# Optimization experiments

Measured on AMD Instinct MI355X. Metric: run time of the kernel, lower is better.

Reference implementation:

```python
import jax, jax.numpy as jnp
import numpy as np

SINK_MAX = 128  # max materialized sink tokens (atten_sink counts are < 64)
NEG_INF = -1e30


def _gather_paged(kv, block_table, pos):
    """Gather tokens from a paged KV cache.
    kv: [num_blocks, block_size, 2, Hkv, D]; block_table: [B, max_blocks] int;
    pos: [B, L] token positions (assumed clipped to valid range).
    Returns [B, L, 2, Hkv, D]."""
    nb, bs = kv.shape[0], kv.shape[1]
    B = pos.shape[0]
    blk = jnp.take_along_axis(block_table, pos // bs, axis=1)  # [B, L]
    flat_idx = blk * bs + pos % bs                              # [B, L]
    kv_flat = kv.reshape(nb * bs, *kv.shape[2:])
    return kv_flat[flat_idx]


def setup_inputs() -> dict:
    key = jax.random.key(0)
    ks = jax.random.split(key, 6)
    B, H, Hkv, D = 32, 32, 4, 128
    NB, BS, NBC = 2048, 128, 512
    MAX_BLK, MAX_CBLK, NSEL = 64, 16, 256
    query = jax.random.normal(ks[0], (B, H, D), dtype=jnp.float32)
    ori_kv = jax.random.normal(ks[1], (NB, BS, 2, Hkv, D), dtype=jnp.float32)
    cmp_kv = jax.random.normal(ks[2], (NBC, BS, 2, Hkv, D), dtype=jnp.float32)
    ori_block_table = (jnp.arange(B * MAX_BLK) % NB).reshape(B, MAX_BLK).astype(jnp.int32)
    cmp_block_table = (jnp.arange(B * MAX_CBLK) % NBC).reshape(B, MAX_CBLK).astype(jnp.int32)
    atten_sink = jax.random.randint(ks[3], (B,), 1, 64, dtype=jnp.int32)
    seqused_kv = jax.random.randint(ks[4], (B,), 4096, 8192, dtype=jnp.int32)
    cmp_sparse_indices = jnp.sort(jax.random.randint(ks[5], (B, NSEL), 0, 1024, dtype=jnp.int32), axis=1)
    return {
        'query_npu': query,
        'q_act_seqs_npu': jnp.ones((B,), dtype=jnp.int32),
        'ori_kv_npu': ori_kv,
        'cmp_kv_npu': cmp_kv,
        'ori_block_table_npu': ori_block_table,
        'cmp_block_table_npu': cmp_block_table,
        'atten_sink_npu': atten_sink,
        'seqused_kv_npu': seqused_kv,
        'cmp_sparse_indices_npu': cmp_sparse_indices,
        'softmax_scale': float(1.0 / np.sqrt(D)),
        'win_size': 512,
        'cmp_ratio': 4,
    }


def reference(query_npu, q_act_seqs_npu, ori_kv_npu, cmp_kv_npu,
              ori_block_table_npu, cmp_block_table_npu, atten_sink_npu,
              seqused_kv_npu, cmp_sparse_indices_npu, softmax_scale,
              win_size, cmp_ratio):
    B, H, D = query_npu.shape
    Hkv = ori_kv_npu.shape[3]
    G = H // Hkv
    bs = ori_kv_npu.shape[1]
    seq = seqused_kv_npu[:, None].astype(jnp.int32)          # [B,1]
    sink = atten_sink_npu[:, None].astype(jnp.int32)         # [B,1]

    # --- sink tokens (first atten_sink tokens of the original cache) ---
    pos_s = jnp.broadcast_to(jnp.arange(SINK_MAX, dtype=jnp.int32)[None, :], (B, SINK_MAX))
    mask_s = (pos_s < sink) & (pos_s < seq)
    kv_s = _gather_paged(ori_kv_npu, ori_block_table_npu, jnp.clip(pos_s, 0))

    # --- sliding window (last win_size original tokens, excluding sink overlap) ---
    pos_w = seq - win_size + jnp.arange(win_size, dtype=jnp.int32)[None, :]
    mask_w = (pos_w >= 0) & (pos_w >= sink)
    kv_w = _gather_paged(ori_kv_npu, ori_block_table_npu, jnp.clip(pos_w, 0))

    # --- sparse-selected compressed tokens ---
    cmp_len = seq // cmp_ratio
    idx_c = cmp_sparse_indices_npu.astype(jnp.int32)         # [B, NSEL]
    mask_c = idx_c < cmp_len
    kv_c = _gather_paged(cmp_kv_npu, cmp_block_table_npu, jnp.clip(idx_c, 0))

    # --- combine all KV sources: [B, L, 2, Hkv, D] ---
    kv = jnp.concatenate([kv_s, kv_w, kv_c], axis=1)
    k, v = kv[:, :, 0], kv[:, :, 1]                           # [B, L, Hkv, D]
    mask = jnp.concatenate([mask_s, mask_w, mask_c], axis=1)  # [B, L]

    # --- GQA attention: heads grouped per kv head ---
    q = query_npu.reshape(B, Hkv, G, D)
    logits = jnp.einsum('bkgd,blkd->bkgl', q, k) * softmax_scale
    logits = jnp.where(mask[:, None, None, :], logits, NEG_INF)
    p = jax.nn.softmax(logits, axis=-1)
    out = jnp.einsum('bkgl,blkd->bkgd', p, v)
    return out.reshape(B, H, D)
```

## Files before the change

kernel.cpp:

```cpp
#include <hip/hip_runtime.h>

constexpr int B_    = 32;
constexpr int H_    = 32;
constexpr int HKV_  = 4;
constexpr int G_    = 8;
constexpr int D_    = 128;
constexpr int BS_   = 128;
constexpr int MAXBLK_  = 64;
constexpr int MAXCBLK_ = 16;
constexpr int NSEL_    = 256;
constexpr int SINKMAX_ = 128;
constexpr int WIN_     = 512;
constexpr int P_       = 8;
constexpr float MSHIFT = 24.0f;

template <int CTRL>
__device__ __forceinline__ float dpp_mov(float x) {
  return __int_as_float(__builtin_amdgcn_update_dpp(
      0, __float_as_int(x), CTRL, 0xF, 0xF, true));
}
constexpr int DPP_XOR1 = 0xB1;
constexpr int DPP_XOR2 = 0x4E;
constexpr int DPP_XOR8 = 0x128;
template <int PATT>
__device__ __forceinline__ float swz_add(float x) {
  return x + __int_as_float(
      __builtin_amdgcn_ds_swizzle(__float_as_int(x), PATT));
}

__global__ __launch_bounds__(256, 4) void sfa_partial_kernel(
    const float* __restrict__ q,
    const float* __restrict__ ori_kv,
    const float* __restrict__ cmp_kv,
    const int*   __restrict__ ori_bt,
    const int*   __restrict__ cmp_bt,
    const int*   __restrict__ sinkp,
    const int*   __restrict__ seqp,
    const int*   __restrict__ selp,
    const float* __restrict__ scalep,
    const int*   __restrict__ ratiop,
    float* __restrict__ o_out,
    float* __restrict__ s_out)
{
  const int part = blockIdx.x;
  const int kh   = blockIdx.y;
  const int b    = blockIdx.z;
  const int tid  = threadIdx.x;
  const int grp  = tid >> 5;
  const int j    = tid & 31;
  const int wave = tid >> 6;
  const int lane = tid & 63;
  const int h    = ((j & 1) << 2) | (j & 2) | ((j >> 3) & 1);
  const bool wr8 = ((j & 20) == 0);

  const float scale = scalep[0];
  const int ratio   = ratiop[0];
  const int seq     = seqp[b];
  const int sink    = sinkp[b];
  const int cmp_len = seq / ratio;

  const int sbt0 = ori_bt[b * MAXBLK_];
  int wbase = seq - WIN_; if (wbase < 0) wbase = 0;
  const int w0 = wbase >> 7;
  auto obt = [&](int k) { int w = w0 + k; if (w > MAXBLK_ - 1) w = MAXBLK_ - 1;
                          return ori_bt[b * MAXBLK_ + w]; };
  const int wb0 = obt(0), wb1 = obt(1), wb2 = obt(2), wb3 = obt(3), wb4 = obt(4);
  const int cb0 = cmp_bt[b * MAXCBLK_ + 0], cb1 = cmp_bt[b * MAXCBLK_ + 1];
  const int cb2 = cmp_bt[b * MAXCBLK_ + 2], cb3 = cmp_bt[b * MAXCBLK_ + 3];
  const int cb4 = cmp_bt[b * MAXCBLK_ + 4], cb5 = cmp_bt[b * MAXCBLK_ + 5];
  const int cb6 = cmp_bt[b * MAXCBLK_ + 6], cb7 = cmp_bt[b * MAXCBLK_ + 7];

  float4 qf[G_];
  const float* qb = q + ((size_t)b * H_ + (size_t)kh * G_) * D_ + 4 * j;
#pragma unroll
  for (int g = 0; g < G_; ++g) qf[g] = *(const float4*)(qb + g * D_);

  float  s_acc = 0.f;
  float4 oacc[G_];
#pragma unroll
  for (int m = 0; m < G_; ++m) oacc[m] = make_float4(0.f, 0.f, 0.f, 0.f);

  int s_end = sink; if (s_end < 0) s_end = 0; if (s_end > SINKMAX_) s_end = SINKMAX_;
  const int sB0 = s_end;
  const int sC0 = s_end + WIN_;
  const int L   = s_end + WIN_ + NSEL_;
  const int chunk = (L + P_ - 1) / P_;
  const int lo = part * chunk;
  int hi = lo + chunk; if (hi > L) hi = L;
  const int cf = sC0 + (((lo + grp) - sC0) & 7);
  const int sel_l = selp[b * NSEL_ + (cf - sC0) + 8 * j];

  auto process = [&](const float4 kf, const float4 vf, const float msk) {
    float lg[G_];
#pragma unroll
    for (int g = 0; g < G_; ++g)
      lg[g] = qf[g].x * kf.x + qf[g].y * kf.y + qf[g].z * kf.z + qf[g].w * kf.w;
    const bool p0 = j & 1, p1 = j & 2, p3 = j & 8;
    float s4[4];
#pragma unroll
    for (int i4 = 0; i4 < 4; ++i4) {
      const float keep = p0 ? lg[4 + i4] : lg[i4];
      const float send = p0 ? lg[i4]     : lg[4 + i4];
      s4[i4] = keep + dpp_mov<DPP_XOR1>(send);
    }
    float s2[2];
#pragma unroll
    for (int i2 = 0; i2 < 2; ++i2) {
      const float keep = p1 ? s4[2 + i2] : s4[i2];
      const float send = p1 ? s4[i2]     : s4[2 + i2];
      s2[i2] = keep + dpp_mov<DPP_XOR2>(send);
    }
    const float keep = p3 ? s2[1] : s2[0];
    const float send = p3 ? s2[0] : s2[1];
    float v1 = keep + dpp_mov<DPP_XOR8>(send);
    v1 = swz_add<0x101F>(v1);
    v1 = swz_add<0x401F>(v1);
    const float e = __expf(fminf(fmaf(v1, scale, -MSHIFT), 80.f)) * msk;
    s_acc += e;
    const float pm1 = dpp_mov<DPP_XOR8>(e);
    const float pm2 = dpp_mov<DPP_XOR2>(e);
    const float pm3 = dpp_mov<DPP_XOR2>(pm1);
    const float pm4 = dpp_mov<DPP_XOR1>(e);
    const float pm5 = dpp_mov<DPP_XOR1>(pm1);
    const float pm6 = dpp_mov<DPP_XOR1>(pm2);
    const float pm7 = dpp_mov<DPP_XOR1>(pm3);
    oacc[0].x += e   * vf.x; oacc[0].y += e   * vf.y; oacc[0].z += e   * vf.z; oacc[0].w += e   * vf.w;
    oacc[1].x += pm1 * vf.x; oacc[1].y += pm1 * vf.y; oacc[1].z += pm1 * vf.z; oacc[1].w += pm1 * vf.w;
    oacc[2].x += pm2 * vf.x; oacc[2].y += pm2 * vf.y; oacc[2].z += pm2 * vf.z; oacc[2].w += pm2 * vf.w;
    oacc[3].x += pm3 * vf.x; oacc[3].y += pm3 * vf.y; oacc[3].z += pm3 * vf.z; oacc[3].w += pm3 * vf.w;
    oacc[4].x += pm4 * vf.x; oacc[4].y += pm4 * vf.y; oacc[4].z += pm4 * vf.z; oacc[4].w += pm4 * vf.w;
    oacc[5].x += pm5 * vf.x; oacc[5].y += pm5 * vf.y; oacc[5].z += pm5 * vf.z; oacc[5].w += pm5 * vf.w;
    oacc[6].x += pm6 * vf.x; oacc[6].y += pm6 * vf.y; oacc[6].z += pm6 * vf.z; oacc[6].w += pm6 * vf.w;
    oacc[7].x += pm7 * vf.x; oacc[7].y += pm7 * vf.y; oacc[7].z += pm7 * vf.z; oacc[7].w += pm7 * vf.w;
  };

#define SEG_LOOP(S0X, S1X, ADDR_CODE)                                          \
  {                                                                            \
    const int s0q = (S0X), s1q = (S1X);                                        \
    int iq = s0q + ((lo + grp - s0q) & 7);                                     \
    if (iq < s1q) {                                                            \
      const float* kbC; float mC;                                              \
      { const int ti = iq; const float* akb; float amsk; ADDR_CODE;            \
        kbC = akb; mC = amsk; }                                                \
      float4 kfC = *(const float4*)(kbC + 4 * j);                              \
      float4 vfC = *(const float4*)(kbC + HKV_ * D_ + 4 * j);                  \
      for (; iq < s1q; iq += 8) {                                              \
        int inq = iq + 8; if (inq >= s1q) inq = s1q - 1;                       \
        const float* kbN; float mN;                                            \
        { const int ti = inq; const float* akb; float amsk; ADDR_CODE;         \
          kbN = akb; mN = amsk; }                                              \
        const float4 kfN = *(const float4*)(kbN + 4 * j);                      \
        const float4 vfN = *(const float4*)(kbN + HKV_ * D_ + 4 * j);          \
        process(kfC, vfC, mC);                                                 \
        kfC = kfN; vfC = vfN; mC = mN;                                         \
      }                                                                        \
    }                                                                          \
  }

  SEG_LOOP(lo, (hi < sB0 ? hi : sB0), {
    amsk = (ti < seq) ? 1.f : 0.f;
    akb = ori_kv + (((size_t)(sbt0 * BS_ + ti)) << 10) + kh * D_;
  });

  SEG_LOOP((lo > sB0 ? lo : sB0), (hi < sC0 ? hi : sC0), {
    const int pos = seq - WIN_ + (ti - sB0);
    amsk = (pos >= 0 && pos >= sink) ? 1.f : 0.f;
    const int pc = pos > 0 ? pos : 0;
    const int wi = (pc >> 7) - w0;
    int blk = wb0;
    blk = (wi == 1) ? wb1 : blk; blk = (wi == 2) ? wb2 : blk;
    blk = (wi == 3) ? wb3 : blk; blk = (wi == 4) ? wb4 : blk;
    akb = ori_kv + (((size_t)(blk * BS_ + (pc & (BS_ - 1)))) << 10) + kh * D_;
  });

  SEG_LOOP((lo > sC0 ? lo : sC0), hi, {
    int mI = (ti - cf) >> 3; mI = mI < 0 ? 0 : (mI > 31 ? 31 : mI);
    const int idx = __shfl(sel_l, mI, 32);
    amsk = (idx < cmp_len) ? 1.f : 0.f;
    const int pc = idx > 0 ? idx : 0;
    const int ci = pc >> 7;
    int blk = cb0;
    blk = (ci == 1) ? cb1 : blk; blk = (ci == 2) ? cb2 : blk;
    blk = (ci == 3) ? cb3 : blk; blk = (ci == 4) ? cb4 : blk;
    blk = (ci == 5) ? cb5 : blk; blk = (ci == 6) ? cb6 : blk;
    blk = (ci == 7) ? cb7 : blk;
    akb = cmp_kv + (((size_t)(blk * BS_ + (pc & (BS_ - 1)))) << 10) + kh * D_;
  });
#undef SEG_LOOP

  s_acc += __shfl_xor(s_acc, 32, 64);
  float* of = reinterpret_cast<float*>(oacc);
#pragma unroll
  for (int t = 0; t < 32; ++t) of[t] += __shfl_xor(of[t], 32, 64);

  __shared__ float lds_o[4][G_][D_];
  __shared__ float lds_s[4][G_];
  if (lane < 32) {
#pragma unroll
    for (int m = 0; m < G_; ++m)
      *(float4*)&lds_o[wave][h ^ m][4 * j] = oacc[m];
    if (wr8) lds_s[wave][h] = s_acc;
  }
  __syncthreads();

#pragma unroll
  for (int e = tid; e < G_ * D_; e += 256) {
    const int g = e >> 7, d = e & (D_ - 1);
    const float num = lds_o[0][g][d] + lds_o[1][g][d] + lds_o[2][g][d] + lds_o[3][g][d];
    o_out[(((size_t)(b * HKV_ + kh) * P_ + part) * G_ + g) * D_ + d] = num;
  }
  if (tid < G_) {
    s_out[((size_t)(b * HKV_ + kh) * P_ + part) * G_ + tid] =
        lds_s[0][tid] + lds_s[1][tid] + lds_s[2][tid] + lds_s[3][tid];
  }
}

__global__ __launch_bounds__(256) void sfa_combine_kernel(
    const float* __restrict__ op, const float* __restrict__ sp,
    float* __restrict__ out)
{
  const int idx = blockIdx.x * 256 + threadIdx.x;
  const int d  = idx & (D_ - 1);
  const int hh = (idx >> 7) & (H_ - 1);
  const int b  = idx >> 12;
  const int kh = hh >> 3, g = hh & 7;
  float num = 0.f, den = 0.f;
#pragma unroll
  for (int p = 0; p < P_; ++p) {
    num += op[(((size_t)(b * HKV_ + kh) * P_ + p) * G_ + g) * D_ + d];
    den += sp[((size_t)(b * HKV_ + kh) * P_ + p) * G_ + g];
  }
  out[idx] = num / den;
}

extern "C" void kernel_launch(void* const* d_in, const int* in_sizes, int n_in,
                              void* d_out, int out_size, void* d_ws, size_t ws_size,
                              hipStream_t stream) {
  const float* q      = (const float*)d_in[0];
  const float* ori_kv = (const float*)d_in[2];
  const float* cmp_kv = (const float*)d_in[3];
  const int*   ori_bt = (const int*)d_in[4];
  const int*   cmp_bt = (const int*)d_in[5];
  const int*   sinkp  = (const int*)d_in[6];
  const int*   seqp   = (const int*)d_in[7];
  const int*   selp   = (const int*)d_in[8];
  const float* scalep = (const float*)d_in[9];
  const int*   ratiop = (const int*)d_in[11];
  float* out = (float*)d_out;

  float* op = (float*)d_ws;
  float* sp = op + (size_t)P_ * B_ * HKV_ * G_ * D_;

  sfa_partial_kernel<<<dim3(P_, HKV_, B_), 256, 0, stream>>>(
      q, ori_kv, cmp_kv, ori_bt, cmp_bt, sinkp, seqp, selp, scalep, ratiop,
      op, sp);
  sfa_combine_kernel<<<(B_ * H_ * D_) / 256, 256, 0, stream>>>(op, sp, out);
}
```

Baseline: 26.49 us.

## Map one token per full wave with float2 lanes, 512-thread blocks, two-deep prefetch

Restructures the partial kernel so each 64-lane wave handles one token with each lane covering two D elements, instead of 32-lane half-waves covering four. Blocks grow to 512 threads (8 waves) and the split factor drops from 8 to 6 partitions. The load loop now double-buffers two tokens ahead to hide gather latency. This cuts per-thread registers and the cross-half reduction, but adds an extra cross-half shuffle per token and an 8-way LDS reduction.

```diff
diff --git a/kernel.cpp b/kernel.cpp
--- a/kernel.cpp
+++ b/kernel.cpp
@@ -11,7 +11,7 @@
 constexpr int NSEL_    = 256;
 constexpr int SINKMAX_ = 128;
 constexpr int WIN_     = 512;
-constexpr int P_       = 8;
+constexpr int P_       = 6;
 constexpr float MSHIFT = 24.0f;
 
 template <int CTRL>
@@ -28,7 +28,7 @@
       __builtin_amdgcn_ds_swizzle(__float_as_int(x), PATT));
 }
 
-__global__ __launch_bounds__(256, 4) void sfa_partial_kernel(
+__global__ __launch_bounds__(512, 6) void sfa_partial_kernel(
     const float* __restrict__ q,
     const float* __restrict__ ori_kv,
     const float* __restrict__ cmp_kv,
@@ -42,16 +42,16 @@
     float* __restrict__ o_out,
     float* __restrict__ s_out)
 {
+  __shared__ float lds_o[8][G_][D_];
+  __shared__ float lds_s[8][G_];
+
   const int part = blockIdx.x;
   const int kh   = blockIdx.y;
   const int b    = blockIdx.z;
   const int tid  = threadIdx.x;
-  const int grp  = tid >> 5;
-  const int j    = tid & 31;
-  const int wave = tid >> 6;
-  const int lane = tid & 63;
+  const int w    = tid >> 6;
+  const int j    = tid & 63;
   const int h    = ((j & 1) << 2) | (j & 2) | ((j >> 3) & 1);
-  const bool wr8 = ((j & 20) == 0);
 
   const float scale = scalep[0];
   const int ratio   = ratiop[0];
@@ -62,23 +62,13 @@
   const int sbt0 = ori_bt[b * MAXBLK_];
   int wbase = seq - WIN_; if (wbase < 0) wbase = 0;
   const int w0 = wbase >> 7;
-  auto obt = [&](int k) { int w = w0 + k; if (w > MAXBLK_ - 1) w = MAXBLK_ - 1;
-                          return ori_bt[b * MAXBLK_ + w]; };
+  auto obt = [&](int k) { int ww = w0 + k; if (ww > MAXBLK_ - 1) ww = MAXBLK_ - 1;
+                          return ori_bt[b * MAXBLK_ + ww]; };
   const int wb0 = obt(0), wb1 = obt(1), wb2 = obt(2), wb3 = obt(3), wb4 = obt(4);
   const int cb0 = cmp_bt[b * MAXCBLK_ + 0], cb1 = cmp_bt[b * MAXCBLK_ + 1];
   const int cb2 = cmp_bt[b * MAXCBLK_ + 2], cb3 = cmp_bt[b * MAXCBLK_ + 3];
   const int cb4 = cmp_bt[b * MAXCBLK_ + 4], cb5 = cmp_bt[b * MAXCBLK_ + 5];
   const int cb6 = cmp_bt[b * MAXCBLK_ + 6], cb7 = cmp_bt[b * MAXCBLK_ + 7];
-
-  float4 qf[G_];
-  const float* qb = q + ((size_t)b * H_ + (size_t)kh * G_) * D_ + 4 * j;
-#pragma unroll
-  for (int g = 0; g < G_; ++g) qf[g] = *(const float4*)(qb + g * D_);
-
-  float  s_acc = 0.f;
-  float4 oacc[G_];
-#pragma unroll
-  for (int m = 0; m < G_; ++m) oacc[m] = make_float4(0.f, 0.f, 0.f, 0.f);
 
   int s_end = sink; if (s_end < 0) s_end = 0; if (s_end > SINKMAX_) s_end = SINKMAX_;
   const int sB0 = s_end;
@@ -87,14 +77,25 @@
   const int chunk = (L + P_ - 1) / P_;
   const int lo = part * chunk;
   int hi = lo + chunk; if (hi > L) hi = L;
-  const int cf = sC0 + (((lo + grp) - sC0) & 7);
-  const int sel_l = selp[b * NSEL_ + (cf - sC0) + 8 * j];
-
-  auto process = [&](const float4 kf, const float4 vf, const float msk) {
+  const int cf = sC0 + (((lo + w) - sC0) & 7);
+  int sidx = (cf - sC0) + 8 * j; if (sidx > NSEL_ - 1) sidx = NSEL_ - 1;
+  const int sel_l = selp[b * NSEL_ + sidx];
+
+  float2 qf[G_];
+  const float* qb = q + ((size_t)b * H_ + (size_t)kh * G_) * D_ + 2 * j;
+#pragma unroll
+  for (int g = 0; g < G_; ++g) qf[g] = *(const float2*)(qb + g * D_);
+
+  float  s_acc = 0.f;
+  float2 oacc[G_];
+#pragma unroll
+  for (int m = 0; m < G_; ++m) oacc[m] = make_float2(0.f, 0.f);
+
+  auto process = [&](const float2 kf, const float2 vf, const float msk) {
     float lg[G_];
 #pragma unroll
     for (int g = 0; g < G_; ++g)
-      lg[g] = qf[g].x * kf.x + qf[g].y * kf.y + qf[g].z * kf.z + qf[g].w * kf.w;
+      lg[g] = qf[g].x * kf.x + qf[g].y * kf.y;
     const bool p0 = j & 1, p1 = j & 2, p3 = j & 8;
     float s4[4];
 #pragma unroll
@@ -115,6 +116,7 @@
     float v1 = keep + dpp_mov<DPP_XOR8>(send);
     v1 = swz_add<0x101F>(v1);
     v1 = swz_add<0x401F>(v1);
+    v1 += __shfl_xor(v1, 32, 64);
     const float e = __expf(fminf(fmaf(v1, scale, -MSHIFT), 80.f)) * msk;
     s_acc += e;
     const float pm1 = dpp_mov<DPP_XOR8>(e);
@@ -124,46 +126,54 @@
     const float pm5 = dpp_mov<DPP_XOR1>(pm1);
     const float pm6 = dpp_mov<DPP_XOR1>(pm2);
     const float pm7 = dpp_mov<DPP_XOR1>(pm3);
-    oacc[0].x += e   * vf.x; oacc[0].y += e   * vf.y; oacc[0].z += e   * vf.z; oacc[0].w += e   * vf.w;
-    oacc[1].x += pm1 * vf.x; oacc[1].y += pm1 * vf.y; oacc[1].z += pm1 * vf.z; oacc[1].w += pm1 * vf.w;
-    oacc[2].x += pm2 * vf.x; oacc[2].y += pm2 * vf.y; oacc[2].z += pm2 * vf.z; oacc[2].w += pm2 * vf.w;
-    oacc[3].x += pm3 * vf.x; oacc[3].y += pm3 * vf.y; oacc[3].z += pm3 * vf.z; oacc[3].w += pm3 * vf.w;
-    oacc[4].x += pm4 * vf.x; oacc[4].y += pm4 * vf.y; oacc[4].z += pm4 * vf.z; oacc[4].w += pm4 * vf.w;
-    oacc[5].x += pm5 * vf.x; oacc[5].y += pm5 * vf.y; oacc[5].z += pm5 * vf.z; oacc[5].w += pm5 * vf.w;
-    oacc[6].x += pm6 * vf.x; oacc[6].y += pm6 * vf.y; oacc[6].z += pm6 * vf.z; oacc[6].w += pm6 * vf.w;
-    oacc[7].x += pm7 * vf.x; oacc[7].y += pm7 * vf.y; oacc[7].z += pm7 * vf.z; oacc[7].w += pm7 * vf.w;
+    oacc[0].x += e   * vf.x; oacc[0].y += e   * vf.y;
+    oacc[1].x += pm1 * vf.x; oacc[1].y += pm1 * vf.y;
+    oacc[2].x += pm2 * vf.x; oacc[2].y += pm2 * vf.y;
+    oacc[3].x += pm3 * vf.x; oacc[3].y += pm3 * vf.y;
+    oacc[4].x += pm4 * vf.x; oacc[4].y += pm4 * vf.y;
+    oacc[5].x += pm5 * vf.x; oacc[5].y += pm5 * vf.y;
+    oacc[6].x += pm6 * vf.x; oacc[6].y += pm6 * vf.y;
+    oacc[7].x += pm7 * vf.x; oacc[7].y += pm7 * vf.y;
   };
 
 #define SEG_LOOP(S0X, S1X, ADDR_CODE)                                          \
   {                                                                            \
     const int s0q = (S0X), s1q = (S1X);                                        \
-    int iq = s0q + ((lo + grp - s0q) & 7);                                     \
+    int iq = s0q + ((lo + w - s0q) & 7);                                       \
     if (iq < s1q) {                                                            \
-      const float* kbC; float mC;                                              \
-      { const int ti = iq; const float* akb; float amsk; ADDR_CODE;            \
-        kbC = akb; mC = amsk; }                                                \
-      float4 kfC = *(const float4*)(kbC + 4 * j);                              \
-      float4 vfC = *(const float4*)(kbC + HKV_ * D_ + 4 * j);                  \
-      for (; iq < s1q; iq += 8) {                                              \
-        int inq = iq + 8; if (inq >= s1q) inq = s1q - 1;                       \
-        const float* kbN; float mN;                                            \
-        { const int ti = inq; const float* akb; float amsk; ADDR_CODE;         \
-          kbN = akb; mN = amsk; }                                              \
-        const float4 kfN = *(const float4*)(kbN + 4 * j);                      \
-        const float4 vfN = *(const float4*)(kbN + HKV_ * D_ + 4 * j);          \
-        process(kfC, vfC, mC);                                                 \
-        kfC = kfN; vfC = vfN; mC = mN;                                         \
+      float2 kA, vA, kB, vB; float mA, mB;                                     \
+      { const int tic = iq; const float* akb; float amsk; ADDR_CODE;           \
+        kA = *(const float2*)(akb + 2 * j);                                    \
+        vA = *(const float2*)(akb + HKV_ * D_ + 2 * j); mA = amsk; }           \
+      { int t2 = iq + 8; const int tic = t2 < s1q ? t2 : s1q - 1;              \
+        const float* akb; float amsk; ADDR_CODE;                               \
+        kB = *(const float2*)(akb + 2 * j);                                    \
+        vB = *(const float2*)(akb + HKV_ * D_ + 2 * j);                        \
+        mB = (iq + 8 < s1q) ? amsk : 0.f; }                                    \
+      for (; iq < s1q; iq += 16) {                                             \
+        process(kA, vA, mA);                                                   \
+        { int t2 = iq + 16; const int tic = t2 < s1q ? t2 : s1q - 1;           \
+          const float* akb; float amsk; ADDR_CODE;                             \
+          kA = *(const float2*)(akb + 2 * j);                                  \
+          vA = *(const float2*)(akb + HKV_ * D_ + 2 * j);                      \
+          mA = (iq + 16 < s1q) ? amsk : 0.f; }                                 \
+        process(kB, vB, mB);                                                   \
+        { int t2 = iq + 24; const int tic = t2 < s1q ? t2 : s1q - 1;           \
+          const float* akb; float amsk; ADDR_CODE;                             \
+          kB = *(const float2*)(akb + 2 * j);                                  \
+          vB = *(const float2*)(akb + HKV_ * D_ + 2 * j);                      \
+          mB = (iq + 24 < s1q) ? amsk : 0.f; }                                 \
       }                                                                        \
     }                                                                          \
   }
 
   SEG_LOOP(lo, (hi < sB0 ? hi : sB0), {
-    amsk = (ti < seq) ? 1.f : 0.f;
-    akb = ori_kv + (((size_t)(sbt0 * BS_ + ti)) << 10) + kh * D_;
+    amsk = (tic < seq) ? 1.f : 0.f;
+    akb = ori_kv + (((size_t)(sbt0 * BS_ + tic)) << 10) + kh * D_;
   });
 
   SEG_LOOP((lo > sB0 ? lo : sB0), (hi < sC0 ? hi : sC0), {
-    const int pos = seq - WIN_ + (ti - sB0);
+    const int pos = tic + (seq - WIN_ - sB0);
     amsk = (pos >= 0 && pos >= sink) ? 1.f : 0.f;
     const int pc = pos > 0 ? pos : 0;
     const int wi = (pc >> 7) - w0;
@@ -174,8 +184,8 @@
   });
 
   SEG_LOOP((lo > sC0 ? lo : sC0), hi, {
-    int mI = (ti - cf) >> 3; mI = mI < 0 ? 0 : (mI > 31 ? 31 : mI);
-    const int idx = __shfl(sel_l, mI, 32);
+    int mI = (tic - cf) >> 3; mI = mI < 0 ? 0 : (mI > 63 ? 63 : mI);
+    const int idx = __shfl(sel_l, mI, 64);
     amsk = (idx < cmp_len) ? 1.f : 0.f;
     const int pc = idx > 0 ? idx : 0;
     const int ci = pc >> 7;
@@ -188,30 +198,25 @@
   });
 #undef SEG_LOOP
 
-  s_acc += __shfl_xor(s_acc, 32, 64);
-  float* of = reinterpret_cast<float*>(oacc);
-#pragma unroll
-  for (int t = 0; t < 32; ++t) of[t] += __shfl_xor(of[t], 32, 64);
-
-  __shared__ float lds_o[4][G_][D_];
-  __shared__ float lds_s[4][G_];
-  if (lane < 32) {
-#pragma unroll
-    for (int m = 0; m < G_; ++m)
-      *(float4*)&lds_o[wave][h ^ m][4 * j] = oacc[m];
-    if (wr8) lds_s[wave][h] = s_acc;
-  }
+#pragma unroll
+  for (int m = 0; m < G_; ++m)
+    *(float2*)&lds_o[w][h ^ m][2 * j] = oacc[m];
+  if ((j & 52) == 0) lds_s[w][h] = s_acc;
   __syncthreads();
 
 #pragma unroll
-  for (int e = tid; e < G_ * D_; e += 256) {
-    const int g = e >> 7, d = e & (D_ - 1);
-    const float num = lds_o[0][g][d] + lds_o[1][g][d] + lds_o[2][g][d] + lds_o[3][g][d];
+  for (int e2 = tid; e2 < G_ * D_; e2 += 512) {
+    const int g = e2 >> 7, d = e2 & (D_ - 1);
+    float num = 0.f;
+#pragma unroll
+    for (int ww = 0; ww < 8; ++ww) num += lds_o[ww][g][d];
     o_out[(((size_t)(b * HKV_ + kh) * P_ + part) * G_ + g) * D_ + d] = num;
   }
   if (tid < G_) {
-    s_out[((size_t)(b * HKV_ + kh) * P_ + part) * G_ + tid] =
-        lds_s[0][tid] + lds_s[1][tid] + lds_s[2][tid] + lds_s[3][tid];
+    float den = 0.f;
+#pragma unroll
+    for (int ww = 0; ww < 8; ++ww) den += lds_s[ww][tid];
+    s_out[((size_t)(b * HKV_ + kh) * P_ + part) * G_ + tid] = den;
   }
 }
 
@@ -251,7 +256,7 @@
   float* op = (float*)d_ws;
   float* sp = op + (size_t)P_ * B_ * HKV_ * G_ * D_;
 
-  sfa_partial_kernel<<<dim3(P_, HKV_, B_), 256, 0, stream>>>(
+  sfa_partial_kernel<<<dim3(P_, HKV_, B_), 512, 0, stream>>>(
       q, ori_kv, cmp_kv, ori_bt, cmp_bt, sinkp, seqp, selp, scalep, ratiop,
       op, sp);
   sfa_combine_kernel<<<(B_ * H_ * D_) / 256, 256, 0, stream>>>(op, sp, out);
```

Result: slower. 28.29 us (+6.8%).
